# Kernel optimization log

Hardware: AMD Instinct MI355X
Metric: run time of the kernel (lower is better)

The kernel has to match this reference:

```python
import jax, jax.numpy as jnp
import numpy as np

HEAD_SIZE = 64

def setup_inputs() -> dict:
    key = jax.random.key(0)
    k1, k2, k3, k4 = jax.random.split(key, 4)
    B, S, D = 8, 2048, 1024
    scale = 1.0 / np.sqrt(D)
    x = jax.random.normal(k1, (B, S, D), dtype=jnp.float32)
    Wk = jax.random.normal(k2, (D, HEAD_SIZE), dtype=jnp.float32) * scale
    Wq = jax.random.normal(k3, (D, HEAD_SIZE), dtype=jnp.float32) * scale
    Wv = jax.random.normal(k4, (D, HEAD_SIZE), dtype=jnp.float32) * scale
    return {"x": x, "Wk": Wk, "Wq": Wq, "Wv": Wv}

def reference(x, Wk, Wq, Wv):
    # x: [B, S, D]; projections to [B, S, H]
    k = jnp.einsum('bsd,dh->bsh', x, Wk)
    q = jnp.einsum('bsd,dh->bsh', x, Wq)
    v = jnp.einsum('bsd,dh->bsh', x, Wv)
    H = q.shape[-1]
    scores = jnp.einsum('bqh,bkh->bqk', q, k) / jnp.sqrt(jnp.float32(H))  # [B,S,S]
    S = scores.shape[-1]
    causal = jnp.tril(jnp.ones((S, S), dtype=bool))
    scores = jnp.where(causal, scores, -jnp.inf)
    attn = jax.nn.softmax(scores, axis=-1)
    z = jnp.einsum('bqk,bkh->bqh', attn, v)  # [B,S,H]
    return z
```

## Files before the change

kernel.cpp:

```cpp
#include <hip/hip_runtime.h>
#include <hip/hip_bf16.h>

#define B_ 8
#define S_ 2048
#define D_ 1024
#define H_ 64

typedef __attribute__((ext_vector_type(8))) short bf16x8;
typedef __attribute__((ext_vector_type(4))) float f32x4;
typedef __attribute__((ext_vector_type(4))) unsigned short u16x4;
typedef unsigned short u16;
typedef unsigned int u32;

#define QSCALE 0.18033688011112042f

static __device__ __forceinline__ u16 f2bf(float f) {
  union { float f; unsigned u; } v; v.f = f;
  unsigned r = v.u + 0x7FFFu + ((v.u >> 16) & 1u);
  return (u16)(r >> 16);
}

__global__ __launch_bounds__(256) void wprep_kernel(const float* __restrict__ Wk,
                                                    const float* __restrict__ Wq,
                                                    const float* __restrict__ Wv,
                                                    u16* __restrict__ Wt) {
  const int c = blockIdx.x;
  const float* W = (c < 64) ? Wq : ((c < 128) ? Wk : Wv);
  const int cc = c & 63;
  for (int d = threadIdx.x; d < D_; d += blockDim.x)
    Wt[c * D_ + d] = f2bf(W[d * H_ + cc]);
}

__global__ __launch_bounds__(256) void qkv_kernel(const float* __restrict__ x,
                                                  const u16* __restrict__ Wt,
                                                  u16* __restrict__ Qb,
                                                  u16* __restrict__ Kb,
                                                  u16* __restrict__ Vt) {
  __shared__ char sh[65536];
  char* const xsb = sh;
  char* const wsb = sh + 16384;

  const int tid = threadIdx.x;
  const int w = tid >> 6;
  const int lane = tid & 63;
  const int r = lane & 15;
  const int g = lane >> 4;
  const int rg = w >> 1;
  const int ch = w & 1;

  const long row0 = (long)blockIdx.x * 32;

#define STAGE_X(kc, buf)                                                       \
  {                                                                            \
    const char* gb = (const char*)x + (size_t)row0 * 4096 + (size_t)(kc) * 256;\
    _Pragma("unroll") for (int j = 0; j < 2; ++j) {                            \
      const int L = j * 4096 + tid * 16;                                       \
      const int row = L >> 8;                                                  \
      const int sw = (L & 255) ^ ((row & 7) << 4);                             \
      __builtin_amdgcn_global_load_lds(                                        \
          (const __attribute__((address_space(1))) u32*)(gb + (size_t)row * 4096 + sw), \
          (__attribute__((address_space(3))) u32*)(xsb + (buf) * 8192 + L),    \
          16, 0, 0);                                                           \
    }                                                                          \
  }

#define STAGE_W(kc, buf)                                                       \
  {                                                                            \
    const char* gb = (const char*)Wt + (size_t)(kc) * 128;                     \
    _Pragma("unroll") for (int j = 0; j < 6; ++j) {                            \
      const int L = j * 4096 + tid * 16;                                       \
      const int col = L >> 7;                                                  \
      const int sw = (L & 127) ^ ((col & 7) << 4);                             \
      __builtin_amdgcn_global_load_lds(                                        \
          (const __attribute__((address_space(1))) u32*)(gb + (size_t)col * 2048 + sw), \
          (__attribute__((address_space(3))) u32*)(wsb + (buf) * 24576 + L),   \
          16, 0, 0);                                                           \
    }                                                                          \
  }

  f32x4 acc[6];
#pragma unroll
  for (int nf = 0; nf < 6; ++nf) acc[nf] = (f32x4){0.f, 0.f, 0.f, 0.f};

  STAGE_X(0, 0);
  STAGE_W(0, 0);
  int cur = 0;

  const int rr = rg * 16 + r;
  const int xswz = (rr & 7) << 4;

  for (int kc = 0; kc < 16; ++kc) {
    __syncthreads();
    if (kc < 15) {
      STAGE_X(kc + 1, cur ^ 1);
      STAGE_W(kc + 1, cur ^ 1);
    }
    __builtin_amdgcn_sched_barrier(0);

    const char* xb = xsb + cur * 8192;
    const char* wb = wsb + cur * 24576;
#pragma unroll
    for (int ks = 0; ks < 2; ++ks) {
      const int cb = ks * 128 + g * 32;
      const float4 lo = *(const float4*)(xb + rr * 256 + (cb ^ xswz));
      const float4 hi = *(const float4*)(xb + rr * 256 + ((cb + 16) ^ xswz));
      bf16x8 a;
      a[0] = (short)f2bf(lo.x); a[1] = (short)f2bf(lo.y);
      a[2] = (short)f2bf(lo.z); a[3] = (short)f2bf(lo.w);
      a[4] = (short)f2bf(hi.x); a[5] = (short)f2bf(hi.y);
      a[6] = (short)f2bf(hi.z); a[7] = (short)f2bf(hi.w);
#pragma unroll
      for (int nf = 0; nf < 6; ++nf) {
        const int col = ch * 96 + nf * 16 + r;
        const int wcb = (ks * 64 + g * 16) ^ ((col & 7) << 4);
        const bf16x8 b = *(const bf16x8*)(wb + col * 128 + wcb);
        acc[nf] = __builtin_amdgcn_mfma_f32_16x16x32_bf16(a, b, acc[nf], 0, 0, 0);
      }
    }
    cur ^= 1;
  }
#undef STAGE_W
#undef STAGE_X

  const int bb = (int)(row0 >> 11);
  const int srow = (int)(row0 & 2047) + rg * 16;
#pragma unroll
  for (int nf = 0; nf < 6; ++nf) {
    const int col = ch * 96 + nf * 16 + r;
    if (col < 64) {
#pragma unroll
      for (int ii = 0; ii < 4; ++ii)
        Qb[(row0 + rg * 16 + 4 * g + ii) * H_ + col] = f2bf(acc[nf][ii] * QSCALE);
    } else if (col < 128) {
#pragma unroll
      for (int ii = 0; ii < 4; ++ii)
        Kb[(row0 + rg * 16 + 4 * g + ii) * H_ + (col - 64)] = f2bf(acc[nf][ii]);
    } else {
      u16x4 vp;
#pragma unroll
      for (int ii = 0; ii < 4; ++ii) vp[ii] = f2bf(acc[nf][ii]);
      *(u16x4*)(Vt + ((size_t)(bb * H_ + (col - 128))) * S_ + srow + 4 * g) = vp;
    }
  }
}

__global__ __launch_bounds__(256, 2) void attn7_kernel(const u16* __restrict__ Qb,
                                                       const u16* __restrict__ Kb,
                                                       const u16* __restrict__ Vt,
                                                       float* __restrict__ out) {
  __shared__ u16 plds[4][16 * 72];
  __shared__ float plo[4][16][68];
  __shared__ float pml[4][2][16];

  const int b = blockIdx.x >> 6;
  const int j = blockIdx.x & 63;
  const int w = threadIdx.x >> 6;
  const int lane = threadIdx.x & 63;
  const int r = lane & 15;
  const int g = lane >> 4;

  const int qt = (w < 2) ? j : (127 - j);
  const int s = w & 1;
  const int q0 = qt << 4;
  const int T = (qt >> 2) + 1;
  const int half = (T + 1) >> 1;
  const int start = s ? half : 0;
  const int end = s ? T : half;

  const u16* Qp = Qb + ((long)(b * S_ + q0 + r)) * H_ + 8 * g;
  const bf16x8 bq0 = *(const bf16x8*)Qp;
  const bf16x8 bq1 = *(const bf16x8*)(Qp + 32);

  const u16* Kbase = Kb + (long)b * S_ * H_ + (long)r * H_ + 8 * g;
  const u16* Vbase = Vt + (long)b * H_ * S_ + (long)r * S_ + 8 * g;

  f32x4 o[4];
#pragma unroll
  for (int nf = 0; nf < 4; ++nf) o[nf] = (f32x4){0.f, 0.f, 0.f, 0.f};
  float m = -INFINITY, l = 0.f;

  u16* pw = plds[w];

  bf16x8 ka[8];
  if (start < end) {
    const int k0 = start << 6;
#pragma unroll
    for (int kf = 0; kf < 4; ++kf) {
      const u16* Kp = Kbase + (long)(k0 + kf * 16) * H_;
      ka[2 * kf] = *(const bf16x8*)(Kp);
      ka[2 * kf + 1] = *(const bf16x8*)(Kp + 32);
    }
  }

  for (int kt = start; kt < end; ++kt) {
    const int k0 = kt << 6;

    f32x4 t4[4];
#pragma unroll
    for (int kf = 0; kf < 4; ++kf) {
      f32x4 t = (f32x4){0.f, 0.f, 0.f, 0.f};
      t = __builtin_amdgcn_mfma_f32_16x16x32_bf16(ka[2 * kf], bq0, t, 0, 0, 0);
      t = __builtin_amdgcn_mfma_f32_16x16x32_bf16(ka[2 * kf + 1], bq1, t, 0, 0, 0);
      t4[kf] = t;
    }

    bf16x8 vv[8];
#pragma unroll
    for (int nf = 0; nf < 4; ++nf) {
      const u16* Vp = Vbase + (long)(nf * 16) * S_ + k0;
      vv[2 * nf] = *(const bf16x8*)(Vp);
      vv[2 * nf + 1] = *(const bf16x8*)(Vp + 32);
    }
    if (kt + 1 < end) {
      const int kn = (kt + 1) << 6;
#pragma unroll
      for (int kf = 0; kf < 4; ++kf) {
        const u16* Kp = Kbase + (long)(kn + kf * 16) * H_;
        ka[2 * kf] = *(const bf16x8*)(Kp);
        ka[2 * kf + 1] = *(const bf16x8*)(Kp + 32);
      }
    }

    if (kt == T - 1) {
#pragma unroll
      for (int kf = 0; kf < 4; ++kf)
#pragma unroll
        for (int i = 0; i < 4; ++i) {
          const int k = k0 + kf * 16 + 4 * g + i;
          if (k > q0 + r) t4[kf][i] = -INFINITY;
        }
    }

    float pm = t4[0][0];
#pragma unroll
    for (int kf = 0; kf < 4; ++kf)
#pragma unroll
      for (int i = 0; i < 4; ++i) pm = fmaxf(pm, t4[kf][i]);
    pm = fmaxf(pm, __shfl_xor(pm, 16));
    pm = fmaxf(pm, __shfl_xor(pm, 32));

    if (__any(pm > m + 8.f)) {
      const float mn = fmaxf(m, pm);
      const float sc = exp2f(m - mn);
      m = mn;
      l *= sc;
      float scr[4];
#pragma unroll
      for (int i = 0; i < 4; ++i) scr[i] = __shfl(sc, 4 * g + i);
#pragma unroll
      for (int nf = 0; nf < 4; ++nf)
#pragma unroll
        for (int i = 0; i < 4; ++i) o[nf][i] *= scr[i];
    }

    float ps = 0.f;
#pragma unroll
    for (int kf = 0; kf < 4; ++kf)
#pragma unroll
      for (int i = 0; i < 4; ++i) {
        const float p = exp2f(t4[kf][i] - m);
        t4[kf][i] = p;
        ps += p;
      }
    ps += __shfl_xor(ps, 16);
    ps += __shfl_xor(ps, 32);
    l += ps;

#pragma unroll
    for (int kf = 0; kf < 4; ++kf) {
      u16x4 pk;
#pragma unroll
      for (int i = 0; i < 4; ++i) pk[i] = f2bf(t4[kf][i]);
      *(u16x4*)(pw + r * 72 + kf * 16 + 4 * g) = pk;
    }

    const bf16x8 pa0 = *(const bf16x8*)(pw + r * 72 + 8 * g);
    const bf16x8 pa1 = *(const bf16x8*)(pw + r * 72 + 32 + 8 * g);

#pragma unroll
    for (int nf = 0; nf < 4; ++nf) {
      o[nf] = __builtin_amdgcn_mfma_f32_16x16x32_bf16(pa0, vv[2 * nf], o[nf], 0, 0, 0);
      o[nf] = __builtin_amdgcn_mfma_f32_16x16x32_bf16(pa1, vv[2 * nf + 1], o[nf], 0, 0, 0);
    }
  }

#pragma unroll
  for (int nf = 0; nf < 4; ++nf)
#pragma unroll
    for (int i = 0; i < 4; ++i)
      plo[w][4 * g + i][nf * 16 + r] = o[nf][i];
  if (g == 0) {
    pml[w][0][r] = m;
    pml[w][1][r] = l;
  }
  __syncthreads();

  const int base = (w >> 1) << 1;
  const int hlf = w & 1;
  const int qq0 = ((base == 0) ? j : (127 - j)) << 4;
#pragma unroll
  for (int rr = 0; rr < 8; ++rr) {
    const int row = hlf * 8 + rr;
    const float mA = pml[base][0][row], mB = pml[base + 1][0][row];
    const float lA = pml[base][1][row], lB = pml[base + 1][1][row];
    const float M = fmaxf(mA, mB);
    const float ea = exp2f(mA - M), eb = exp2f(mB - M);
    const float inv = 1.f / (lA * ea + lB * eb);
    const float oo = plo[base][row][lane] * ea + plo[base + 1][row][lane] * eb;
    out[((long)(b * S_ + qq0 + row)) * H_ + lane] = oo * inv;
  }
}

extern "C" void kernel_launch(void* const* d_in, const int* in_sizes, int n_in,
                              void* d_out, int out_size, void* d_ws, size_t ws_size,
                              hipStream_t stream) {
  const float* x  = (const float*)d_in[0];
  const float* Wk = (const float*)d_in[1];
  const float* Wq = (const float*)d_in[2];
  const float* Wv = (const float*)d_in[3];
  float* out = (float*)d_out;

  u16* Qb = (u16*)d_ws;
  u16* Kb = Qb + (long)B_ * S_ * H_;
  u16* Vt = Kb + (long)B_ * S_ * H_;
  u16* Wt = Vt + (long)B_ * S_ * H_;

  wprep_kernel<<<192, 256, 0, stream>>>(Wk, Wq, Wv, Wt);
  qkv_kernel<<<512, 256, 0, stream>>>(x, Wt, Qb, Kb, Vt);
  attn7_kernel<<<B_ * 64, 256, 0, stream>>>(Qb, Kb, Vt, out);
}
```

Before: 65.12 us.

## Split causal KV range four ways per query tile with 512-thread blocks

The attention kernel grows from 4 to 8 waves per block, so each of the two paired query tiles has its KV tiles split across four waves instead of two. The final merge now combines four partial (m, l, o) states per row and writes with vectorized float4 stores. The aim is shorter per-wave serial KV loops and more parallelism for the 512-block grid. In exchange it doubles LDS use per block and adds merge overhead, and the launch bounds no longer request two blocks per CU, which may reduce occupancy.

```diff
diff --git a/kernel.cpp b/kernel.cpp
--- a/kernel.cpp
+++ b/kernel.cpp
@@ -144,13 +144,13 @@
   }
 }
 
-__global__ __launch_bounds__(256, 2) void attn7_kernel(const u16* __restrict__ Qb,
-                                                       const u16* __restrict__ Kb,
-                                                       const u16* __restrict__ Vt,
-                                                       float* __restrict__ out) {
-  __shared__ u16 plds[4][16 * 72];
-  __shared__ float plo[4][16][68];
-  __shared__ float pml[4][2][16];
+__global__ __launch_bounds__(512) void attn8_kernel(const u16* __restrict__ Qb,
+                                                    const u16* __restrict__ Kb,
+                                                    const u16* __restrict__ Vt,
+                                                    float* __restrict__ out) {
+  __shared__ u16 plds[8][16 * 72];
+  __shared__ float plo[8][16][68];
+  __shared__ float pml[8][2][16];
 
   const int b = blockIdx.x >> 6;
   const int j = blockIdx.x & 63;
@@ -158,14 +158,14 @@
   const int lane = threadIdx.x & 63;
   const int r = lane & 15;
   const int g = lane >> 4;
-
-  const int qt = (w < 2) ? j : (127 - j);
-  const int s = w & 1;
+  const int grp = w >> 2;
+  const int qr = w & 3;
+
+  const int qt = grp ? (127 - j) : j;
   const int q0 = qt << 4;
   const int T = (qt >> 2) + 1;
-  const int half = (T + 1) >> 1;
-  const int start = s ? half : 0;
-  const int end = s ? T : half;
+  const int start = (qr * T) >> 2;
+  const int end = ((qr + 1) * T) >> 2;
 
   const u16* Qp = Qb + ((long)(b * S_ + q0 + r)) * H_ + 8 * g;
   const bf16x8 bq0 = *(const bf16x8*)Qp;
@@ -295,20 +295,25 @@
   }
   __syncthreads();
 
-  const int base = (w >> 1) << 1;
-  const int hlf = w & 1;
-  const int qq0 = ((base == 0) ? j : (127 - j)) << 4;
-#pragma unroll
-  for (int rr = 0; rr < 8; ++rr) {
-    const int row = hlf * 8 + rr;
-    const float mA = pml[base][0][row], mB = pml[base + 1][0][row];
-    const float lA = pml[base][1][row], lB = pml[base + 1][1][row];
-    const float M = fmaxf(mA, mB);
-    const float ea = exp2f(mA - M), eb = exp2f(mB - M);
-    const float inv = 1.f / (lA * ea + lB * eb);
-    const float oo = plo[base][row][lane] * ea + plo[base + 1][row][lane] * eb;
-    out[((long)(b * S_ + qq0 + row)) * H_ + lane] = oo * inv;
-  }
+  const int lw = w & 3;
+  const int base = (w >> 2) << 2;
+  const int row = (lw << 2) + g;
+  const int c0 = r << 2;
+  const int qq0 = ((w >> 2) ? (127 - j) : j) << 4;
+  const float m0 = pml[base][0][row], m1 = pml[base + 1][0][row];
+  const float m2 = pml[base + 2][0][row], m3 = pml[base + 3][0][row];
+  const float M = fmaxf(fmaxf(m0, m1), fmaxf(m2, m3));
+  const float e0 = exp2f(m0 - M), e1 = exp2f(m1 - M);
+  const float e2 = exp2f(m2 - M), e3 = exp2f(m3 - M);
+  const float L = pml[base][1][row] * e0 + pml[base + 1][1][row] * e1 +
+                  pml[base + 2][1][row] * e2 + pml[base + 3][1][row] * e3;
+  const float inv = 1.f / L;
+  f32x4 os;
+#pragma unroll
+  for (int c = 0; c < 4; ++c)
+    os[c] = (plo[base][row][c0 + c] * e0 + plo[base + 1][row][c0 + c] * e1 +
+             plo[base + 2][row][c0 + c] * e2 + plo[base + 3][row][c0 + c] * e3) * inv;
+  *(f32x4*)(out + ((long)(b * S_ + qq0 + row)) * H_ + c0) = os;
 }
 
 extern "C" void kernel_launch(void* const* d_in, const int* in_sizes, int n_in,
@@ -327,5 +332,5 @@
 
   wprep_kernel<<<192, 256, 0, stream>>>(Wk, Wq, Wv, Wt);
   qkv_kernel<<<512, 256, 0, stream>>>(x, Wt, Qb, Kb, Vt);
-  attn7_kernel<<<B_ * 64, 256, 0, stream>>>(Qb, Kb, Vt, out);
-}
+  attn8_kernel<<<B_ * 64, 512, 0, stream>>>(Qb, Kb, Vt, out);
+}
```

Result: no change. 66.28 us (+1.8%).

## Keep QKV weights in registers with persistent blocks; prefetch V in attention

Applied to the files above, without the earlier changes.

The QKV projection kernel now loads each wave's weight slice into registers once. Blocks loop over four 16-row chunks of x, staged into large double-buffered LDS tiles, with the K dimension split across two wave groups and reduced through LDS. This removes the repeated per-chunk weight staging, at the cost of heavy register and LDS use that lowers occupancy. The attention kernel also prefetches the next V tile alongside the next K tile to hide load latency.

```diff
diff --git a/kernel.cpp b/kernel.cpp
--- a/kernel.cpp
+++ b/kernel.cpp
@@ -31,117 +31,114 @@
     Wt[c * D_ + d] = f2bf(W[d * H_ + cc]);
 }
 
-__global__ __launch_bounds__(256) void qkv_kernel(const float* __restrict__ x,
-                                                  const u16* __restrict__ Wt,
-                                                  u16* __restrict__ Qb,
-                                                  u16* __restrict__ Kb,
-                                                  u16* __restrict__ Vt) {
-  __shared__ char sh[65536];
-  char* const xsb = sh;
-  char* const wsb = sh + 16384;
+__global__ __launch_bounds__(512, 2) void qkv_kernel(const float* __restrict__ x,
+                                                     const u16* __restrict__ Wt,
+                                                     u16* __restrict__ Qb,
+                                                     u16* __restrict__ Kb,
+                                                     u16* __restrict__ Vt) {
+  __shared__ char xs[2][65536];
+  __shared__ float red[4][64][12];
 
   const int tid = threadIdx.x;
+  const int lane = tid & 63;
   const int w = tid >> 6;
-  const int lane = tid & 63;
   const int r = lane & 15;
   const int g = lane >> 4;
-  const int rg = w >> 1;
-  const int ch = w & 1;
-
-  const long row0 = (long)blockIdx.x * 32;
-
-#define STAGE_X(kc, buf)                                                       \
+  const int cg = w & 3;
+  const int ks = w >> 2;
+
+#define STAGE_X(chunk, buf)                                                    \
   {                                                                            \
-    const char* gb = (const char*)x + (size_t)row0 * 4096 + (size_t)(kc) * 256;\
-    _Pragma("unroll") for (int j = 0; j < 2; ++j) {                            \
-      const int L = j * 4096 + tid * 16;                                       \
-      const int row = L >> 8;                                                  \
-      const int sw = (L & 255) ^ ((row & 7) << 4);                             \
+    const char* gb = (const char*)x + (size_t)(chunk) * 65536;                 \
+    _Pragma("unroll") for (int j = 0; j < 8; ++j) {                            \
+      const int L = j * 8192 + tid * 16;                                       \
+      const int row = L >> 12;                                                 \
+      const int off = (L & 4095) ^ ((row & 7) << 4);                           \
       __builtin_amdgcn_global_load_lds(                                        \
-          (const __attribute__((address_space(1))) u32*)(gb + (size_t)row * 4096 + sw), \
-          (__attribute__((address_space(3))) u32*)(xsb + (buf) * 8192 + L),    \
+          (const __attribute__((address_space(1))) u32*)(gb + (size_t)row * 4096 + off), \
+          (__attribute__((address_space(3))) u32*)(&xs[buf][0] + L),           \
           16, 0, 0);                                                           \
     }                                                                          \
   }
 
-#define STAGE_W(kc, buf)                                                       \
-  {                                                                            \
-    const char* gb = (const char*)Wt + (size_t)(kc) * 128;                     \
-    _Pragma("unroll") for (int j = 0; j < 6; ++j) {                            \
-      const int L = j * 4096 + tid * 16;                                       \
-      const int col = L >> 7;                                                  \
-      const int sw = (L & 127) ^ ((col & 7) << 4);                             \
-      __builtin_amdgcn_global_load_lds(                                        \
-          (const __attribute__((address_space(1))) u32*)(gb + (size_t)col * 2048 + sw), \
-          (__attribute__((address_space(3))) u32*)(wsb + (buf) * 24576 + L),   \
-          16, 0, 0);                                                           \
-    }                                                                          \
-  }
-
-  f32x4 acc[6];
-#pragma unroll
-  for (int nf = 0; nf < 6; ++nf) acc[nf] = (f32x4){0.f, 0.f, 0.f, 0.f};
-
-  STAGE_X(0, 0);
-  STAGE_W(0, 0);
+  STAGE_X(blockIdx.x, 0);
+
+  const u16* wbase = Wt + (size_t)(cg * 48 + r) * D_ + ks * 512 + g * 8;
+  bf16x8 wf[3][16];
+#pragma unroll
+  for (int nf = 0; nf < 3; ++nf)
+#pragma unroll
+    for (int s = 0; s < 16; ++s)
+      wf[nf][s] = *(const bf16x8*)(wbase + (size_t)nf * 16 * D_ + s * 32);
+
   int cur = 0;
-
-  const int rr = rg * 16 + r;
-  const int xswz = (rr & 7) << 4;
-
-  for (int kc = 0; kc < 16; ++kc) {
-    __syncthreads();
-    if (kc < 15) {
-      STAGE_X(kc + 1, cur ^ 1);
-      STAGE_W(kc + 1, cur ^ 1);
-    }
+  const int rsw = (r & 7) << 4;
+
+  for (int i = 0; i < 4; ++i) {
+    const long row0 = ((long)blockIdx.x + (long)i * 256) * 16;
+
+    asm volatile("s_waitcnt vmcnt(0)" ::: "memory");
     __builtin_amdgcn_sched_barrier(0);
-
-    const char* xb = xsb + cur * 8192;
-    const char* wb = wsb + cur * 24576;
-#pragma unroll
-    for (int ks = 0; ks < 2; ++ks) {
-      const int cb = ks * 128 + g * 32;
-      const float4 lo = *(const float4*)(xb + rr * 256 + (cb ^ xswz));
-      const float4 hi = *(const float4*)(xb + rr * 256 + ((cb + 16) ^ xswz));
+    __builtin_amdgcn_s_barrier();
+    if (i < 3) STAGE_X(blockIdx.x + (i + 1) * 256, cur ^ 1);
+    __builtin_amdgcn_sched_barrier(0);
+
+    const char* xb = &xs[cur][0];
+    f32x4 a0 = (f32x4){0.f, 0.f, 0.f, 0.f};
+    f32x4 a1 = a0, a2 = a0;
+#pragma unroll
+    for (int s = 0; s < 16; ++s) {
+      const int c0 = ks * 2048 + s * 128 + g * 32;
+      const float4 lo = *(const float4*)(xb + r * 4096 + (c0 ^ rsw));
+      const float4 hi = *(const float4*)(xb + r * 4096 + ((c0 + 16) ^ rsw));
       bf16x8 a;
       a[0] = (short)f2bf(lo.x); a[1] = (short)f2bf(lo.y);
       a[2] = (short)f2bf(lo.z); a[3] = (short)f2bf(lo.w);
       a[4] = (short)f2bf(hi.x); a[5] = (short)f2bf(hi.y);
       a[6] = (short)f2bf(hi.z); a[7] = (short)f2bf(hi.w);
-#pragma unroll
-      for (int nf = 0; nf < 6; ++nf) {
-        const int col = ch * 96 + nf * 16 + r;
-        const int wcb = (ks * 64 + g * 16) ^ ((col & 7) << 4);
-        const bf16x8 b = *(const bf16x8*)(wb + col * 128 + wcb);
-        acc[nf] = __builtin_amdgcn_mfma_f32_16x16x32_bf16(a, b, acc[nf], 0, 0, 0);
+      a0 = __builtin_amdgcn_mfma_f32_16x16x32_bf16(a, wf[0][s], a0, 0, 0, 0);
+      a1 = __builtin_amdgcn_mfma_f32_16x16x32_bf16(a, wf[1][s], a1, 0, 0, 0);
+      a2 = __builtin_amdgcn_mfma_f32_16x16x32_bf16(a, wf[2][s], a2, 0, 0, 0);
+    }
+
+    if (ks == 1) {
+      float* dst = &red[cg][lane][0];
+      *(f32x4*)&dst[0] = a0; *(f32x4*)&dst[4] = a1; *(f32x4*)&dst[8] = a2;
+    }
+    asm volatile("s_waitcnt lgkmcnt(0)" ::: "memory");
+    __builtin_amdgcn_sched_barrier(0);
+    __builtin_amdgcn_s_barrier();
+    if (ks == 0) {
+      const float* src = &red[cg][lane][0];
+      a0 += *(const f32x4*)&src[0];
+      a1 += *(const f32x4*)&src[4];
+      a2 += *(const f32x4*)&src[8];
+
+      const int bb = (int)(row0 >> 11);
+      const int srow = (int)(row0 & 2047);
+      f32x4 sv[3] = {a0, a1, a2};
+#pragma unroll
+      for (int nf = 0; nf < 3; ++nf) {
+        const int col = cg * 48 + nf * 16 + r;
+        if (col < 64) {
+#pragma unroll
+          for (int ii = 0; ii < 4; ++ii)
+            Qb[(row0 + 4 * g + ii) * H_ + col] = f2bf(sv[nf][ii] * QSCALE);
+        } else if (col < 128) {
+#pragma unroll
+          for (int ii = 0; ii < 4; ++ii)
+            Kb[(row0 + 4 * g + ii) * H_ + (col - 64)] = f2bf(sv[nf][ii]);
+        } else {
+          u16x4 vp;
+#pragma unroll
+          for (int ii = 0; ii < 4; ++ii) vp[ii] = f2bf(sv[nf][ii]);
+          *(u16x4*)(Vt + ((size_t)(bb * H_ + (col - 128))) * S_ + srow + 4 * g) = vp;
+        }
       }
     }
     cur ^= 1;
   }
-#undef STAGE_W
 #undef STAGE_X
-
-  const int bb = (int)(row0 >> 11);
-  const int srow = (int)(row0 & 2047) + rg * 16;
-#pragma unroll
-  for (int nf = 0; nf < 6; ++nf) {
-    const int col = ch * 96 + nf * 16 + r;
-    if (col < 64) {
-#pragma unroll
-      for (int ii = 0; ii < 4; ++ii)
-        Qb[(row0 + rg * 16 + 4 * g + ii) * H_ + col] = f2bf(acc[nf][ii] * QSCALE);
-    } else if (col < 128) {
-#pragma unroll
-      for (int ii = 0; ii < 4; ++ii)
-        Kb[(row0 + rg * 16 + 4 * g + ii) * H_ + (col - 64)] = f2bf(acc[nf][ii]);
-    } else {
-      u16x4 vp;
-#pragma unroll
-      for (int ii = 0; ii < 4; ++ii) vp[ii] = f2bf(acc[nf][ii]);
-      *(u16x4*)(Vt + ((size_t)(bb * H_ + (col - 128))) * S_ + srow + 4 * g) = vp;
-    }
-  }
 }
 
 __global__ __launch_bounds__(256, 2) void attn7_kernel(const u16* __restrict__ Qb,
@@ -181,7 +178,7 @@
 
   u16* pw = plds[w];
 
-  bf16x8 ka[8];
+  bf16x8 ka[8], vv[8], vn[8];
   if (start < end) {
     const int k0 = start << 6;
 #pragma unroll
@@ -189,6 +186,9 @@
       const u16* Kp = Kbase + (long)(k0 + kf * 16) * H_;
       ka[2 * kf] = *(const bf16x8*)(Kp);
       ka[2 * kf + 1] = *(const bf16x8*)(Kp + 32);
+      const u16* Vp = Vbase + (long)(kf * 16) * S_ + k0;
+      vv[2 * kf] = *(const bf16x8*)(Vp);
+      vv[2 * kf + 1] = *(const bf16x8*)(Vp + 32);
     }
   }
 
@@ -204,13 +204,6 @@
       t4[kf] = t;
     }
 
-    bf16x8 vv[8];
-#pragma unroll
-    for (int nf = 0; nf < 4; ++nf) {
-      const u16* Vp = Vbase + (long)(nf * 16) * S_ + k0;
-      vv[2 * nf] = *(const bf16x8*)(Vp);
-      vv[2 * nf + 1] = *(const bf16x8*)(Vp + 32);
-    }
     if (kt + 1 < end) {
       const int kn = (kt + 1) << 6;
 #pragma unroll
@@ -218,6 +211,9 @@
         const u16* Kp = Kbase + (long)(kn + kf * 16) * H_;
         ka[2 * kf] = *(const bf16x8*)(Kp);
         ka[2 * kf + 1] = *(const bf16x8*)(Kp + 32);
+        const u16* Vp = Vbase + (long)(kf * 16) * S_ + kn;
+        vn[2 * kf] = *(const bf16x8*)(Vp);
+        vn[2 * kf + 1] = *(const bf16x8*)(Vp + 32);
       }
     }
 
@@ -281,6 +277,11 @@
     for (int nf = 0; nf < 4; ++nf) {
       o[nf] = __builtin_amdgcn_mfma_f32_16x16x32_bf16(pa0, vv[2 * nf], o[nf], 0, 0, 0);
       o[nf] = __builtin_amdgcn_mfma_f32_16x16x32_bf16(pa1, vv[2 * nf + 1], o[nf], 0, 0, 0);
+    }
+
+    if (kt + 1 < end) {
+#pragma unroll
+      for (int q = 0; q < 8; ++q) vv[q] = vn[q];
     }
   }
 
@@ -326,6 +327,6 @@
   u16* Wt = Vt + (long)B_ * S_ * H_;
 
   wprep_kernel<<<192, 256, 0, stream>>>(Wk, Wq, Wv, Wt);
-  qkv_kernel<<<512, 256, 0, stream>>>(x, Wt, Qb, Kb, Vt);
+  qkv_kernel<<<256, 512, 0, stream>>>(x, Wt, Qb, Kb, Vt);
   attn7_kernel<<<B_ * 64, 256, 0, stream>>>(Qb, Kb, Vt, out);
 }
```

Measured after the change: 84.86 us. 1.3x slower.
